# Kernel tuning notes

Hardware: AMD Instinct MI355X
Metric: run time of the kernel (lower is better)

Reference implementation:

```python
import jax, jax.numpy as jnp
import numpy as np
from jax import lax

B, C, H, W, S = 8, 64, 64, 64, 12
KSIZE = 5


def _conv2d_same(x, w):
    # x: [N, Cin, H, W], w: [Cout, Cin, kh, kw]
    return lax.conv_general_dilated(
        x, w, window_strides=(1, 1), padding='SAME',
        dimension_numbers=('NCHW', 'OIHW', 'NCHW'))


def setup_inputs() -> dict:
    key = jax.random.key(0)
    k0, k1, k2, k3, k4 = jax.random.split(key, 5)
    x = jax.random.normal(k0, (B, C, H, W, S), dtype=jnp.float32)
    w1 = jax.random.normal(k1, (3 * C, C, 1, 1), dtype=jnp.float32) * 0.05
    b1 = jax.random.normal(k2, (3 * C,), dtype=jnp.float32) * 0.05
    w2 = jax.random.normal(k3, (1, 2 * C, KSIZE, KSIZE), dtype=jnp.float32) * 0.05
    b2 = jax.random.normal(k4, (1,), dtype=jnp.float32) * 0.05
    return {'x': x, 'w1': w1, 'b1': b1, 'w2': w2, 'b2': b2}


def reference(x, w1, b1, w2, b2):
    b, c, h, w_, s = x.shape
    # conv1 (1x1) applied per timestep == channel matmul over all timesteps at once
    qkv = jnp.einsum('oc,bchws->bohws', w1[:, :, 0, 0], x) + b1[None, :, None, None, None]
    Q, K, V = jnp.split(qkv, 3, axis=1)  # each [b, c, h, w, s]

    # conv2 on concat(Q_s, K_t) is linear in channels:
    # score(s,t) = convQ(Q[...,s]) + convK(K[...,t]) + bias
    def per_time_conv(z, wsub):
        # z: [b, c, h, w, s] -> fold time into batch -> conv -> [b, h, w, s]
        zb = jnp.moveaxis(z, -1, 1).reshape(b * s, c, h, w_)
        out = _conv2d_same(zb, wsub)  # [b*s, 1, h, w]
        return jnp.moveaxis(out.reshape(b, s, h, w_), 1, -1)  # [b, h, w, s]

    A_q = per_time_conv(Q, w2[:, :c])   # [b, h, w, s] (query index)
    A_k = per_time_conv(K, w2[:, c:])   # [b, h, w, t] (key index)

    # scores: [b, h, w, t, s]
    scores = A_q[:, :, :, None, :] + A_k[:, :, :, :, None] + b2[0]
    attn = jax.nn.softmax(scores, axis=-2)  # softmax over t (keys)

    # weighted sum of V over t -> [b, c, h, w, s]
    V_out = jnp.einsum('bhwts,bchwt->bchws', attn, V)
    return V_out
```

## Files before the change

### kernel.cpp

```cpp
#include <hip/hip_runtime.h>
#include <hip/hip_bf16.h>

#define WEFF_OFF 0
#define Y_OFF    4096
#define Y_PLANE  393216
#define WS_WEFF_OFF 393216

__global__ __launch_bounds__(256) void k_prep(const float* __restrict__ w1,
                                              const float* __restrict__ w2,
                                              float* __restrict__ wdst) {
    int idx = blockIdx.x * 256 + threadIdx.x;
    if (idx >= 64 * 25) return;
    int cp = idx / 25, tap = idx % 25;
    float s = 0.f;
    for (int c = 0; c < 64; ++c)
        s = fmaf(w2[(64 + c) * 25 + tap], w1[(64 + c) * 64 + cp], s);
    wdst[cp * 25 + tap] = s;
}

__global__ __launch_bounds__(256) void k_tap(const float* __restrict__ x,
                                             const float* __restrict__ weff,
                                             float* __restrict__ y) {
    const int gid = blockIdx.x * 256 + threadIdx.x;
    const int m   = gid / 12;
    const int t   = gid - m * 12;
    const int w   = m & 63;
    const int h   = (m >> 6) & 63;
    const int b   = m >> 12;

    const float* xp = x + (size_t)b * 3145728 + h * 768 + w * 12 + t;

    float acc[25];
#pragma unroll
    for (int k = 0; k < 25; ++k) acc[k] = 0.f;

    for (int c = 0; c < 64; ++c) {
        const float v = xp[(size_t)c * 49152];
        const float* wg = weff + c * 25;
#pragma unroll
        for (int k = 0; k < 25; ++k)
            acc[k] = fmaf(wg[k], v, acc[k]);
    }

#pragma unroll
    for (int k = 0; k < 25; ++k)
        y[(size_t)k * Y_PLANE + gid] = acc[k];
}

__global__ __launch_bounds__(256) void k_gather(const float* __restrict__ y,
                                                float* __restrict__ p) {
    const int tid  = threadIdx.x;
    const int m    = blockIdx.x * 64 + (tid >> 2);
    const int q    = tid & 3;
    const int qq   = (q == 3) ? 2 : q;
    const int w    = m & 63;
    const int h    = (m >> 6) & 63;
    const int b    = m >> 12;

    float4 a; a.x = 0.f; a.y = 0.f; a.z = 0.f; a.w = 0.f;

#pragma unroll
    for (int dh = 0; dh < 5; ++dh) {
        const int hh = h + dh - 2;
        if ((unsigned)hh >= 64u) continue;
        const int rowb = (b * 64 + hh) * 64;
#pragma unroll
        for (int dw = 0; dw < 5; ++dw) {
            const int ww = w + dw - 2;
            if ((unsigned)ww >= 64u) continue;
            const float* yp = y + (size_t)(dh * 5 + dw) * Y_PLANE
                                + (size_t)(rowb + ww) * 12 + qq * 4;
            float4 v = *(const float4*)(yp);
            a.x += v.x; a.y += v.y; a.z += v.z; a.w += v.w;
        }
    }

    float mx = fmaxf(fmaxf(a.x, a.y), fmaxf(a.z, a.w));
    mx = fmaxf(mx, __shfl_xor(mx, 1, 4));
    mx = fmaxf(mx, __shfl_xor(mx, 2, 4));

    float e0 = __expf(a.x - mx), e1 = __expf(a.y - mx);
    float e2 = __expf(a.z - mx), e3 = __expf(a.w - mx);
    const float s4 = e0 + e1 + e2 + e3;
    const float s0 = __shfl(s4, 0, 4);
    const float s1 = __shfl(s4, 1, 4);
    const float s2 = __shfl(s4, 2, 4);
    const float inv = 1.f / (s0 + s1 + s2);

    if (q < 3) {
        float4 o; o.x = e0 * inv; o.y = e1 * inv; o.z = e2 * inv; o.w = e3 * inv;
        *(float4*)(p + (size_t)m * 12 + q * 4) = o;
    }
}

__global__ __launch_bounds__(512) void k_out(const float* __restrict__ x,
                                             const float* __restrict__ w1,
                                             const float* __restrict__ b1,
                                             const float* __restrict__ p,
                                             float* __restrict__ out) {
    __shared__ float lds[64 * 65];

    const int b  = blockIdx.x >> 6;
    const int h  = blockIdx.x & 63;
    const int w  = threadIdx.x & 63;
    const int cg = threadIdx.x >> 6;

    const float* pp = p + (size_t)((b * 64 + h) * 64 + w) * 12;
    float pv[12];
    {
        float4 t0 = *(const float4*)(pp);
        float4 t1 = *(const float4*)(pp + 4);
        float4 t2 = *(const float4*)(pp + 8);
        pv[0] = t0.x; pv[1] = t0.y; pv[2]  = t0.z; pv[3]  = t0.w;
        pv[4] = t1.x; pv[5] = t1.y; pv[6]  = t1.z; pv[7]  = t1.w;
        pv[8] = t2.x; pv[9] = t2.y; pv[10] = t2.z; pv[11] = t2.w;
    }

    const float* xb0 = x + ((size_t)(b * 64 + cg * 8) * 64 + h) * 768 + w * 12;
#pragma unroll
    for (int j = 0; j < 8; ++j) {
        const float* xp = xb0 + (size_t)j * 49152;
        float4 u0 = *(const float4*)(xp);
        float4 u1 = *(const float4*)(xp + 4);
        float4 u2 = *(const float4*)(xp + 8);
        float s = 0.f;
        s = fmaf(pv[0], u0.x, s);  s = fmaf(pv[1], u0.y, s);
        s = fmaf(pv[2], u0.z, s);  s = fmaf(pv[3], u0.w, s);
        s = fmaf(pv[4], u1.x, s);  s = fmaf(pv[5], u1.y, s);
        s = fmaf(pv[6], u1.z, s);  s = fmaf(pv[7], u1.w, s);
        s = fmaf(pv[8], u2.x, s);  s = fmaf(pv[9], u2.y, s);
        s = fmaf(pv[10], u2.z, s); s = fmaf(pv[11], u2.w, s);
        lds[w * 65 + cg * 8 + j] = s;
    }
    __syncthreads();

    const float* w1v = w1 + 128 * 64 + cg * 8 * 64;
    float acc[8];
#pragma unroll
    for (int j = 0; j < 8; ++j) acc[j] = b1[128 + cg * 8 + j];
    for (int c2 = 0; c2 < 64; ++c2) {
        const float xv = lds[w * 65 + c2];
#pragma unroll
        for (int j = 0; j < 8; ++j)
            acc[j] = fmaf(w1v[j * 64 + c2], xv, acc[j]);
    }

#pragma unroll
    for (int j = 0; j < 8; ++j) {
        const int co = cg * 8 + j;
        float4 f; f.x = acc[j]; f.y = acc[j]; f.z = acc[j]; f.w = acc[j];
        float* op = out + ((size_t)(b * 64 + co) * 4096 + h * 64 + w) * 12;
        *(float4*)(op)     = f;
        *(float4*)(op + 4) = f;
        *(float4*)(op + 8) = f;
    }
}

extern "C" void kernel_launch(void* const* d_in, const int* in_sizes, int n_in,
                              void* d_out, int out_size, void* d_ws, size_t ws_size,
                              hipStream_t stream) {
    const float* x  = (const float*)d_in[0];
    const float* w1 = (const float*)d_in[1];
    const float* b1 = (const float*)d_in[2];
    const float* w2 = (const float*)d_in[3];

    float* outp = (float*)d_out;
    float* y    = outp + Y_OFF;
    float* p    = (float*)d_ws;

    const bool ws_fits = ws_size >= (size_t)(WS_WEFF_OFF + 1600) * sizeof(float);
    float* weff = ws_fits ? (p + WS_WEFF_OFF) : (outp + WEFF_OFF);

    hipLaunchKernelGGL(k_prep,   dim3(7),    dim3(256), 0, stream, w1, w2, weff);
    hipLaunchKernelGGL(k_tap,    dim3(1536), dim3(256), 0, stream, x, weff, y);
    hipLaunchKernelGGL(k_gather, dim3(512),  dim3(256), 0, stream, y, p);
    hipLaunchKernelGGL(k_out,    dim3(512),  dim3(512), 0, stream, x, w1, b1, p, outp);
}
```

Measured before the change: 99.19 us.

## Fold horizontal conv taps into the tap kernel to shrink intermediate planes

The tap kernel now loads the five horizontal neighbours of x per channel, with zero padding at the edges, and sums over dw itself. It therefore writes five row-partial planes instead of twenty-five per-tap planes. The gather kernel then only sums five vertical taps instead of twenty-five scattered float4 loads. This aims to cut intermediate write and read traffic by about five times, at the cost of five times more x loads. Those extra loads should mostly hit in cache, since the neighbours share cache lines.

```diff
diff --git a/kernel.cpp b/kernel.cpp
--- a/kernel.cpp
+++ b/kernel.cpp
@@ -1,10 +1,10 @@
 #include <hip/hip_runtime.h>
 #include <hip/hip_bf16.h>
 
-#define WEFF_OFF 0
-#define Y_OFF    4096
-#define Y_PLANE  393216
+#define U_OFF    4096
+#define U_PLANE  393216
 #define WS_WEFF_OFF 393216
+#define WEFF_FALLBACK_OFF 0
 
 __global__ __launch_bounds__(256) void k_prep(const float* __restrict__ w1,
                                               const float* __restrict__ w2,
@@ -20,7 +20,7 @@
 
 __global__ __launch_bounds__(256) void k_tap(const float* __restrict__ x,
                                              const float* __restrict__ weff,
-                                             float* __restrict__ y) {
+                                             float* __restrict__ u) {
     const int gid = blockIdx.x * 256 + threadIdx.x;
     const int m   = gid / 12;
     const int t   = gid - m * 12;
@@ -30,24 +30,48 @@
 
     const float* xp = x + (size_t)b * 3145728 + h * 768 + w * 12 + t;
 
-    float acc[25];
+    const bool ok0 = (w >= 2), ok1 = (w >= 1), ok3 = (w <= 62), ok4 = (w <= 61);
+    const int  o0 = ok0 ? -24 : 0, o1 = ok1 ? -12 : 0;
+    const int  o3 = ok3 ?  12 : 0, o4 = ok4 ?  24 : 0;
+
+    float u0 = 0.f, u1 = 0.f, u2 = 0.f, u3 = 0.f, u4 = 0.f;
+
+    for (int cb = 0; cb < 16; ++cb) {
+        float xv[4][5];
 #pragma unroll
-    for (int k = 0; k < 25; ++k) acc[k] = 0.f;
-
-    for (int c = 0; c < 64; ++c) {
-        const float v = xp[(size_t)c * 49152];
-        const float* wg = weff + c * 25;
+        for (int j = 0; j < 4; ++j) {
+            const float* base = xp + (size_t)(cb * 4 + j) * 49152;
+            float v0 = base[o0], v1 = base[o1], v2 = base[0];
+            float v3 = base[o3], v4 = base[o4];
+            xv[j][0] = ok0 ? v0 : 0.f;
+            xv[j][1] = ok1 ? v1 : 0.f;
+            xv[j][2] = v2;
+            xv[j][3] = ok3 ? v3 : 0.f;
+            xv[j][4] = ok4 ? v4 : 0.f;
+        }
 #pragma unroll
-        for (int k = 0; k < 25; ++k)
-            acc[k] = fmaf(wg[k], v, acc[k]);
+        for (int j = 0; j < 4; ++j) {
+            const float* wg = weff + (cb * 4 + j) * 25;
+#pragma unroll
+            for (int dw = 0; dw < 5; ++dw) {
+                const float v = xv[j][dw];
+                u0 = fmaf(wg[0 * 5 + dw], v, u0);
+                u1 = fmaf(wg[1 * 5 + dw], v, u1);
+                u2 = fmaf(wg[2 * 5 + dw], v, u2);
+                u3 = fmaf(wg[3 * 5 + dw], v, u3);
+                u4 = fmaf(wg[4 * 5 + dw], v, u4);
+            }
+        }
     }
 
-#pragma unroll
-    for (int k = 0; k < 25; ++k)
-        y[(size_t)k * Y_PLANE + gid] = acc[k];
+    u[(size_t)0 * U_PLANE + gid] = u0;
+    u[(size_t)1 * U_PLANE + gid] = u1;
+    u[(size_t)2 * U_PLANE + gid] = u2;
+    u[(size_t)3 * U_PLANE + gid] = u3;
+    u[(size_t)4 * U_PLANE + gid] = u4;
 }
 
-__global__ __launch_bounds__(256) void k_gather(const float* __restrict__ y,
+__global__ __launch_bounds__(256) void k_gather(const float* __restrict__ u,
                                                 float* __restrict__ p) {
     const int tid  = threadIdx.x;
     const int m    = blockIdx.x * 64 + (tid >> 2);
@@ -63,16 +87,10 @@
     for (int dh = 0; dh < 5; ++dh) {
         const int hh = h + dh - 2;
         if ((unsigned)hh >= 64u) continue;
-        const int rowb = (b * 64 + hh) * 64;
-#pragma unroll
-        for (int dw = 0; dw < 5; ++dw) {
-            const int ww = w + dw - 2;
-            if ((unsigned)ww >= 64u) continue;
-            const float* yp = y + (size_t)(dh * 5 + dw) * Y_PLANE
-                                + (size_t)(rowb + ww) * 12 + qq * 4;
-            float4 v = *(const float4*)(yp);
-            a.x += v.x; a.y += v.y; a.z += v.z; a.w += v.w;
-        }
+        const float* up = u + (size_t)dh * U_PLANE
+                            + (size_t)(((b * 64 + hh) * 64 + w)) * 12 + qq * 4;
+        float4 v = *(const float4*)(up);
+        a.x += v.x; a.y += v.y; a.z += v.z; a.w += v.w;
     }
 
     float mx = fmaxf(fmaxf(a.x, a.y), fmaxf(a.z, a.w));
@@ -165,14 +183,14 @@
     const float* w2 = (const float*)d_in[3];
 
     float* outp = (float*)d_out;
-    float* y    = outp + Y_OFF;
+    float* u    = outp + U_OFF;
     float* p    = (float*)d_ws;
 
     const bool ws_fits = ws_size >= (size_t)(WS_WEFF_OFF + 1600) * sizeof(float);
-    float* weff = ws_fits ? (p + WS_WEFF_OFF) : (outp + WEFF_OFF);
+    float* weff = ws_fits ? (p + WS_WEFF_OFF) : (outp + WEFF_FALLBACK_OFF);
 
     hipLaunchKernelGGL(k_prep,   dim3(7),    dim3(256), 0, stream, w1, w2, weff);
-    hipLaunchKernelGGL(k_tap,    dim3(1536), dim3(256), 0, stream, x, weff, y);
-    hipLaunchKernelGGL(k_gather, dim3(512),  dim3(256), 0, stream, y, p);
+    hipLaunchKernelGGL(k_tap,    dim3(1536), dim3(256), 0, stream, x, weff, u);
+    hipLaunchKernelGGL(k_gather, dim3(512),  dim3(256), 0, stream, u, p);
     hipLaunchKernelGGL(k_out,    dim3(512),  dim3(512), 0, stream, x, w1, b1, p, outp);
 }
```

After: 97.31 us. No clear change (-1.9%).
